# Performance work log

Hardware: AMD Instinct MI355X
Metric: run time of the kernel (lower is better)

Reference implementation:

```python
import jax, jax.numpy as jnp
import numpy as np

DIM = 1024
HEADS = 16
DIM_HEAD = 64
CHUNK = 64
INNER = HEADS * DIM_HEAD  # 1024


def setup_inputs() -> dict:
    key = jax.random.key(0)
    k1, k2, k3 = jax.random.split(key, 3)
    x = jax.random.normal(k1, (4, 4096, DIM), dtype=jnp.float32)
    # nn.Linear weights stored as (out, in); apply as x @ W.T
    w_qkv = jax.random.normal(k2, (INNER * 3, DIM), dtype=jnp.float32) * (DIM ** -0.5)
    w_out = jax.random.normal(k3, (DIM, INNER), dtype=jnp.float32) * (INNER ** -0.5)
    b_out = jnp.zeros((DIM,), dtype=jnp.float32)
    return {"x": x, "w_qkv": w_qkv, "w_out": w_out, "b_out": b_out}


def reference(x, w_qkv, w_out, b_out):
    b, n, _ = x.shape
    scale = DIM_HEAD ** -0.5
    qkv = jnp.einsum('bnd,ed->bne', x, w_qkv)  # (b, n, 3*inner)
    q, k, v = jnp.split(qkv, 3, axis=-1)
    nblk = n // CHUNK

    def to_blocks(t):
        # (b, n, h*d) -> (b, h, nblk, c, d)
        t = t.reshape(b, n, HEADS, DIM_HEAD).transpose(0, 2, 1, 3)
        return t.reshape(b, HEADS, nblk, CHUNK, DIM_HEAD)

    qb, kb, vb = to_blocks(q), to_blocks(k), to_blocks(v)
    scores = jnp.einsum('bhgqd,bhgkd->bhgqk', qb, kb) * scale  # block-local
    attn = jax.nn.softmax(scores, axis=-1)
    ob = jnp.einsum('bhgqk,bhgkd->bhgqd', attn, vb)
    out = ob.reshape(b, HEADS, n, DIM_HEAD).transpose(0, 2, 1, 3).reshape(b, n, INNER)
    return jnp.einsum('bne,de->bnd', out, w_out) + b_out
```

## Files before the change

kernel.cpp:

```cpp
#include <hip/hip_runtime.h>
#include <stdint.h>

typedef __attribute__((ext_vector_type(8))) short bf16x8;
typedef __attribute__((ext_vector_type(4))) float f32x4;

__device__ __forceinline__ unsigned short bf16_of(float f) {
  union { float f; uint32_t u; } x; x.f = f;
  uint32_t r = x.u + 0x7fffu + ((x.u >> 16) & 1u);
  return (unsigned short)(r >> 16);
}

#define GLD16(gp, lp) __builtin_amdgcn_global_load_lds( \
    (const __attribute__((address_space(1))) uint32_t*)(gp), \
    (__attribute__((address_space(3))) uint32_t*)(lp), 16, 0, 0)

#define BAR() do { asm volatile("" ::: "memory"); __builtin_amdgcn_s_barrier(); asm volatile("" ::: "memory"); } while (0)

__global__ void cvt_f32_bf16(const float* __restrict__ src,
                             unsigned short* __restrict__ dst, int n4) {
  int i = blockIdx.x * blockDim.x + threadIdx.x;
  int stride = gridDim.x * blockDim.x;
  for (int j = i; j < n4; j += stride) {
    float4 f = ((const float4*)src)[j];
    union { unsigned short s[4]; uint2 v; } u;
    u.s[0] = bf16_of(f.x); u.s[1] = bf16_of(f.y);
    u.s[2] = bf16_of(f.z); u.s[3] = bf16_of(f.w);
    ((uint2*)dst)[j] = u.v;
  }
}

template<int BIAS, int OUTF32, int GW, int NSEG>
__global__ __launch_bounds__(512, 2)
void gemm256h(const unsigned short* __restrict__ A,
              const unsigned short* __restrict__ B,
              void* __restrict__ C, const float* __restrict__ bias,
              int N, int K)
{
  __shared__ __align__(1024) unsigned short sm[65536];
  char* const smb = (char*)sm;
  const int tid = threadIdx.x, w = tid >> 6, lane = tid & 63;
  const int wm = w >> 2, wn = w & 3;
  const int fr = lane & 15, kg = lane >> 4;
  const int swz = (fr & 7) << 4;
  const int srow = lane >> 3, sslot = lane & 7;
  const int cXcd = blockIdx.x & 7, iIdx = blockIdx.x >> 3;
  const int NT_tot = NSEG * 16;

  auto tileMN = [&](int s, int& mt, int& nt) {
    const int T = cXcd * (32 * NSEG) + s * 32 + iIdx;
    const int g = T / (64 * GW), rr = T % (64 * GW);
    mt = rr / GW; nt = g * GW + rr % GW;
  };

  int stOff[2][2];
  #pragma unroll
  for (int h = 0; h < 2; ++h)
    #pragma unroll
    for (int i2 = 0; i2 < 2; ++i2)
      stOff[h][i2] = (h * 128 + (i2 * 8 + w) * 8 + srow) * K + (sslot ^ srow) * 8;

  int curMt, curNt, nxtMt, nxtNt;
  tileMN(0, curMt, curNt);
  nxtMt = curMt; nxtNt = curNt;
  if (NSEG > 1) tileMN(1, nxtMt, nxtNt);
  const unsigned short* aSeg  = A + ((size_t)curMt << 8) * K;
  const unsigned short* bSeg  = B + ((size_t)curNt << 8) * K;
  const unsigned short* aSegN = A + ((size_t)nxtMt << 8) * K;
  const unsigned short* bSegN = B + ((size_t)nxtNt << 8) * K;

  auto STAGEh = [&](const unsigned short* src, int opnd, int half, int parity) {
    char* region = smb + opnd * 65536 + parity * 32768 + half * 16384;
    GLD16(src + stOff[half][0], region + w * 1024);
    GLD16(src + stOff[half][1], region + (8 + w) * 1024);
  };
  auto LDA = [&](char* Ab, int j, int kk) -> bf16x8 {
    const int r = 32 * j + 16 * wm + fr;
    return *(const bf16x8*)(Ab + r * 128 + ((kk * 64 + kg * 16) ^ swz));
  };
  auto LDB = [&](char* Bb, int l, int kk) -> bf16x8 {
    const int r = 64 * l + 16 * wn + fr;
    return *(const bf16x8*)(Bb + r * 128 + ((kk * 64 + kg * 16) ^ swz));
  };

  f32x4 acc[8][4] = {};

  STAGEh(bSeg, 1, 0, 0);
  STAGEh(aSeg, 0, 0, 0);
  STAGEh(bSeg, 1, 1, 0);
  STAGEh(aSeg, 0, 1, 0);

  for (int s = 0; s < NSEG; ++s) {
    for (int tt = 0; tt < 16; ++tt) {
      const int T = s * 16 + tt;
      char* Ab = smb + (T & 1) * 32768;
      char* Bb = smb + 65536 + (T & 1) * 32768;

      asm volatile("s_waitcnt vmcnt(0)" ::: "memory");
      BAR();

      bf16x8 a[4][2], bb[4][2];
      #pragma unroll
      for (int l = 0; l < 4; ++l) { bb[l][0] = LDB(Bb, l, 0); bb[l][1] = LDB(Bb, l, 1); }
      #pragma unroll
      for (int j = 0; j < 4; ++j) { a[j][0] = LDA(Ab, j, 0); a[j][1] = LDA(Ab, j, 1); }

      if (T + 1 < NT_tot) {
        const int p1 = (T + 1) & 1;
        const unsigned short *aS, *bS;
        if (tt < 15) { aS = aSeg + ((tt + 1) << 6); bS = bSeg + ((tt + 1) << 6); }
        else         { aS = aSegN;                  bS = bSegN; }
        STAGEh(bS, 1, 0, p1);
        STAGEh(aS, 0, 0, p1);
        STAGEh(bS, 1, 1, p1);
        STAGEh(aS, 0, 1, p1);
      }

      __builtin_amdgcn_s_setprio(1);
      #pragma unroll
      for (int kk = 0; kk < 2; ++kk)
        #pragma unroll
        for (int j = 0; j < 4; ++j)
          #pragma unroll
          for (int l = 0; l < 4; ++l)
            acc[j][l] = __builtin_amdgcn_mfma_f32_16x16x32_bf16(a[j][kk], bb[l][kk], acc[j][l], 0, 0, 0);
      __builtin_amdgcn_s_setprio(0);

      #pragma unroll
      for (int j = 0; j < 4; ++j) { a[j][0] = LDA(Ab, j + 4, 0); a[j][1] = LDA(Ab, j + 4, 1); }
      __builtin_amdgcn_s_setprio(1);
      #pragma unroll
      for (int kk = 0; kk < 2; ++kk)
        #pragma unroll
        for (int j = 0; j < 4; ++j)
          #pragma unroll
          for (int l = 0; l < 4; ++l)
            acc[j + 4][l] = __builtin_amdgcn_mfma_f32_16x16x32_bf16(a[j][kk], bb[l][kk], acc[j + 4][l], 0, 0, 0);
      __builtin_amdgcn_s_setprio(0);
    }

    const int bm0 = curMt << 8, bn0 = curNt << 8;
    #pragma unroll
    for (int l = 0; l < 4; ++l) {
      const int col = bn0 + 64 * l + 16 * wn + fr;
      float bb2 = 0.0f;
      if (BIAS && OUTF32) bb2 = bias[col];
      #pragma unroll
      for (int j = 0; j < 8; ++j) {
        const int row0 = bm0 + 32 * j + 16 * wm + kg * 4;
        #pragma unroll
        for (int rr = 0; rr < 4; ++rr) {
          if (OUTF32)
            ((float*)C)[(size_t)(row0 + rr) * N + col] = acc[j][l][rr] + bb2;
          else
            ((unsigned short*)C)[(size_t)(row0 + rr) * N + col] = bf16_of(acc[j][l][rr]);
        }
      }
    }
    #pragma unroll
    for (int j = 0; j < 8; ++j)
      #pragma unroll
      for (int l = 0; l < 4; ++l)
        acc[j][l] = f32x4{0.f, 0.f, 0.f, 0.f};

    curMt = nxtMt; curNt = nxtNt;
    aSeg = aSegN; bSeg = bSegN;
    if (s + 2 < NSEG) {
      tileMN(s + 2, nxtMt, nxtNt);
      aSegN = A + ((size_t)nxtMt << 8) * K;
      bSegN = B + ((size_t)nxtNt << 8) * K;
    }
  }
}

__global__ __launch_bounds__(256, 2)
void attn_block(const unsigned short* __restrict__ qkv,
                unsigned short* __restrict__ o)
{
  __shared__ __align__(1024) unsigned short Qs[64 * 64];
  __shared__ __align__(1024) unsigned short Ks[64 * 64];
  __shared__ __align__(1024) unsigned short Vt[64 * 64];
  __shared__ __align__(1024) unsigned short Ps[64 * 64];
  const int tid = threadIdx.x, w = tid >> 6, lane = tid & 63;
  const int g = blockIdx.x, h = blockIdx.y, b = blockIdx.z;
  const size_t mbase = (size_t)b * 4096 + (size_t)g * 64;
  const unsigned short* qg = qkv + mbase * 3072 + h * 64;
  const unsigned short* kgl = qkv + mbase * 3072 + 1024 + h * 64;
  const unsigned short* vg = qkv + mbase * 3072 + 2048 + h * 64;

  #pragma unroll
  for (int i = 0; i < 2; ++i) {
    const int chunk = i * 4 + w;
    const int row = chunk * 8 + (lane >> 3);
    const int c8 = (lane & 7) ^ (row & 7);
    GLD16(qg + (size_t)row * 3072 + c8 * 8, (char*)Qs + chunk * 1024);
    GLD16(kgl + (size_t)row * 3072 + c8 * 8, (char*)Ks + chunk * 1024);
  }
  #pragma unroll
  for (int i = 0; i < 2; ++i) {
    const int c = i * 256 + tid;
    const int n = c >> 3, d0 = (c & 7) * 8;
    bf16x8 v = *(const bf16x8*)(vg + (size_t)n * 3072 + d0);
    #pragma unroll
    for (int j = 0; j < 8; ++j) {
      const int d = d0 + j;
      const int bo = d * 128 + n * 2;
      *(unsigned short*)((char*)Vt + (bo ^ ((d & 7) << 4))) = (unsigned short)v[j];
    }
  }
  __syncthreads();

  const int fr = lane & 15, kg = lane >> 4;
  f32x4 s[4] = {};
  #pragma unroll
  for (int kt = 0; kt < 2; ++kt) {
    const int kb = kt * 64 + kg * 16;
    const int rq = w * 16 + fr;
    bf16x8 aq = *(const bf16x8*)((const char*)Qs + rq * 128 + (kb ^ ((rq & 7) << 4)));
    #pragma unroll
    for (int nf = 0; nf < 4; ++nf) {
      const int rk = nf * 16 + fr;
      bf16x8 bk = *(const bf16x8*)((const char*)Ks + rk * 128 + (kb ^ ((rk & 7) << 4)));
      s[nf] = __builtin_amdgcn_mfma_f32_16x16x32_bf16(aq, bk, s[nf], 0, 0, 0);
    }
  }

  const float scale = 0.125f;
  float inv[4];
  #pragma unroll
  for (int r = 0; r < 4; ++r) {
    float m0 = fmaxf(fmaxf(s[0][r], s[1][r]), fmaxf(s[2][r], s[3][r]));
    #pragma unroll
    for (int d = 1; d < 16; d <<= 1) m0 = fmaxf(m0, __shfl_xor(m0, d));
    float sum = 0.0f;
    #pragma unroll
    for (int nf = 0; nf < 4; ++nf) {
      float p = __expf((s[nf][r] - m0) * scale);
      s[nf][r] = p;
      sum += p;
    }
    #pragma unroll
    for (int d = 1; d < 16; d <<= 1) sum += __shfl_xor(sum, d);
    inv[r] = 1.0f / sum;
  }

  #pragma unroll
  for (int r = 0; r < 4; ++r) {
    const int m = w * 16 + kg * 4 + r;
    #pragma unroll
    for (int nf = 0; nf < 4; ++nf) {
      const int bo = m * 128 + (nf * 16 + fr) * 2;
      *(unsigned short*)((char*)Ps + (bo ^ ((m & 7) << 4))) = bf16_of(s[nf][r] * inv[r]);
    }
  }
  __syncthreads();

  f32x4 oa[4] = {};
  #pragma unroll
  for (int kt = 0; kt < 2; ++kt) {
    const int kb = kt * 64 + kg * 16;
    const int rp = w * 16 + fr;
    bf16x8 ap = *(const bf16x8*)((const char*)Ps + rp * 128 + (kb ^ ((rp & 7) << 4)));
    #pragma unroll
    for (int df = 0; df < 4; ++df) {
      const int rv = df * 16 + fr;
      bf16x8 bv = *(const bf16x8*)((const char*)Vt + rv * 128 + (kb ^ ((rv & 7) << 4)));
      oa[df] = __builtin_amdgcn_mfma_f32_16x16x32_bf16(ap, bv, oa[df], 0, 0, 0);
    }
  }
  #pragma unroll
  for (int df = 0; df < 4; ++df) {
    #pragma unroll
    for (int r = 0; r < 4; ++r) {
      const size_t row = mbase + w * 16 + kg * 4 + r;
      const int col = h * 64 + df * 16 + fr;
      o[row * 1024 + col] = bf16_of(oa[df][r]);
    }
  }
}

extern "C" void kernel_launch(void* const* d_in, const int* in_sizes, int n_in,
                              void* d_out, int out_size, void* d_ws, size_t ws_size,
                              hipStream_t stream) {
  const float* x     = (const float*)d_in[0];
  const float* w_qkv = (const float*)d_in[1];
  const float* w_out = (const float*)d_in[2];
  const float* b_out = (const float*)d_in[3];
  char* ws = (char*)d_ws;
  const size_t SZ_X  = (size_t)16384 * 1024 * 2;
  const size_t SZ_WQ = (size_t)3072 * 1024 * 2;
  const size_t SZ_WO = (size_t)1024 * 1024 * 2;
  unsigned short* xb  = (unsigned short*)ws;
  unsigned short* wqb = (unsigned short*)(ws + SZ_X);
  unsigned short* wob = (unsigned short*)(ws + SZ_X + SZ_WQ);
  unsigned short* qkv = (unsigned short*)(ws + SZ_X + SZ_WQ + SZ_WO);
  unsigned short* ob  = xb;

  cvt_f32_bf16<<<2048, 256, 0, stream>>>(x, xb, 16384 * 1024 / 4);
  cvt_f32_bf16<<<512, 256, 0, stream>>>(w_qkv, wqb, 3072 * 1024 / 4);
  cvt_f32_bf16<<<256, 256, 0, stream>>>(w_out, wob, 1024 * 1024 / 4);
  gemm256h<0,0,6,3><<<dim3(256), 512, 0, stream>>>(xb, wqb, qkv, nullptr, 3072, 1024);
  attn_block<<<dim3(64, 16, 4), 256, 0, stream>>>(qkv, ob);
  gemm256h<1,1,4,1><<<dim3(256), 512, 0, stream>>>(ob, wob, d_out, b_out, 1024, 1024);
}
```

Before: 179.7 us.

## Merge conversion kernels, stage attention output through LDS, raise occupancy hint

The three f32-to-bf16 conversion launches become one kernel that walks x, w_qkv and w_out with a single grid-stride loop, saving two launches. The attention kernel now writes its output tile to a swizzled LDS buffer, synchronises, and stores it to global memory as 16-byte rows instead of scattered 2-byte writes. Its launch bounds hint goes from 2 to 4 blocks per CU. The extra 8KB of LDS and the added barrier may offset the gain from the wider stores.

```diff
diff --git a/kernel.cpp b/kernel.cpp
--- a/kernel.cpp
+++ b/kernel.cpp
@@ -16,16 +16,24 @@
 
 #define BAR() do { asm volatile("" ::: "memory"); __builtin_amdgcn_s_barrier(); asm volatile("" ::: "memory"); } while (0)
 
-__global__ void cvt_f32_bf16(const float* __restrict__ src,
-                             unsigned short* __restrict__ dst, int n4) {
+__global__ void cvt_all(const float* __restrict__ x, const float* __restrict__ wq,
+                        const float* __restrict__ wo,
+                        unsigned short* __restrict__ xb, unsigned short* __restrict__ wqb,
+                        unsigned short* __restrict__ wob) {
+  const int N_X = 4194304, N_WQ = 786432, N_WO = 262144;
+  const int total = N_X + N_WQ + N_WO;
   int i = blockIdx.x * blockDim.x + threadIdx.x;
   int stride = gridDim.x * blockDim.x;
-  for (int j = i; j < n4; j += stride) {
-    float4 f = ((const float4*)src)[j];
+  for (int j = i; j < total; j += stride) {
+    const float* src; unsigned short* dst; int off;
+    if (j < N_X)            { src = x;  dst = xb;  off = j; }
+    else if (j < N_X + N_WQ){ src = wq; dst = wqb; off = j - N_X; }
+    else                    { src = wo; dst = wob; off = j - N_X - N_WQ; }
+    float4 f = ((const float4*)src)[off];
     union { unsigned short s[4]; uint2 v; } u;
     u.s[0] = bf16_of(f.x); u.s[1] = bf16_of(f.y);
     u.s[2] = bf16_of(f.z); u.s[3] = bf16_of(f.w);
-    ((uint2*)dst)[j] = u.v;
+    ((uint2*)dst)[off] = u.v;
   }
 }
 
@@ -172,7 +180,7 @@
   }
 }
 
-__global__ __launch_bounds__(256, 2)
+__global__ __launch_bounds__(256, 4)
 void attn_block(const unsigned short* __restrict__ qkv,
                 unsigned short* __restrict__ o)
 {
@@ -180,6 +188,7 @@
   __shared__ __align__(1024) unsigned short Ks[64 * 64];
   __shared__ __align__(1024) unsigned short Vt[64 * 64];
   __shared__ __align__(1024) unsigned short Ps[64 * 64];
+  __shared__ __align__(1024) unsigned short Os[64 * 64];
   const int tid = threadIdx.x, w = tid >> 6, lane = tid & 63;
   const int g = blockIdx.x, h = blockIdx.y, b = blockIdx.z;
   const size_t mbase = (size_t)b * 4096 + (size_t)g * 64;
@@ -267,14 +276,27 @@
       oa[df] = __builtin_amdgcn_mfma_f32_16x16x32_bf16(ap, bv, oa[df], 0, 0, 0);
     }
   }
+
   #pragma unroll
   for (int df = 0; df < 4; ++df) {
     #pragma unroll
     for (int r = 0; r < 4; ++r) {
-      const size_t row = mbase + w * 16 + kg * 4 + r;
-      const int col = h * 64 + df * 16 + fr;
-      o[row * 1024 + col] = bf16_of(oa[df][r]);
-    }
+      const int m = w * 16 + kg * 4 + r;
+      const int bo = m * 128 + (df * 16 + fr) * 2;
+      *(unsigned short*)((char*)Os + (bo ^ ((m & 7) << 4))) = bf16_of(oa[df][r]);
+    }
+  }
+  __syncthreads();
+  {
+    const int row = tid >> 2;
+    const int sb = (tid & 3) * 32;
+    const int sw = (row & 7) << 4;
+    char* rp = (char*)Os + row * 128;
+    uint4 v0 = *(uint4*)(rp + (sb ^ sw));
+    uint4 v1 = *(uint4*)(rp + ((sb + 16) ^ sw));
+    char* op = (char*)(o + (mbase + row) * 1024 + h * 64) + sb;
+    *(uint4*)op = v0;
+    *(uint4*)(op + 16) = v1;
   }
 }
 
@@ -295,9 +317,7 @@
   unsigned short* qkv = (unsigned short*)(ws + SZ_X + SZ_WQ + SZ_WO);
   unsigned short* ob  = xb;
 
-  cvt_f32_bf16<<<2048, 256, 0, stream>>>(x, xb, 16384 * 1024 / 4);
-  cvt_f32_bf16<<<512, 256, 0, stream>>>(w_qkv, wqb, 3072 * 1024 / 4);
-  cvt_f32_bf16<<<256, 256, 0, stream>>>(w_out, wob, 1024 * 1024 / 4);
+  cvt_all<<<2048, 256, 0, stream>>>(x, w_qkv, w_out, xb, wqb, wob);
   gemm256h<0,0,6,3><<<dim3(256), 512, 0, stream>>>(xb, wqb, qkv, nullptr, 3072, 1024);
   attn_block<<<dim3(64, 16, 4), 256, 0, stream>>>(qkv, ob);
   gemm256h<1,1,4,1><<<dim3(256), 512, 0, stream>>>(ob, wob, d_out, b_out, 1024, 1024);
```

Measured after the change: 173.5 us, median of 2. 3.4% less time.
